# Kernel tuning notes

Measured on AMD Instinct MI355X. Metric: run time of the kernel, lower is better.

The kernel has to match this reference:

```python
import jax, jax.numpy as jnp
import numpy as np

B, T, C, H = 4, 2048, 1024, 16
D = C // H  # head dim = 64

def setup_inputs() -> dict:
    key = jax.random.key(0)
    k1, k2, k3 = jax.random.split(key, 3)
    x = jax.random.normal(k1, (B, T, C), dtype=jnp.float32)
    # torch Linear weight [out,in]; store transposed for x @ W
    W_attn = jax.random.normal(k2, (C, 3 * C), dtype=jnp.float32) * (1.0 / np.sqrt(C))
    W_proj = jax.random.normal(k3, (C, C), dtype=jnp.float32) * (1.0 / np.sqrt(C))
    return {"x": x, "W_attn": W_attn, "W_proj": W_proj}

def reference(x, W_attn, W_proj):
    qkv = x @ W_attn                          # [B,T,3C]
    q, k, v = jnp.split(qkv, 3, axis=-1)
    # [B,T,C] -> [B,H,T,D]
    def heads(t):
        return t.reshape(B, T, H, D).transpose(0, 2, 1, 3)
    q, k, v = heads(q), heads(k), heads(v)
    att = jnp.einsum('bhqd,bhkd->bhqk', q, k) * (1.0 / np.sqrt(D))  # [B,H,T,T]
    causal = jnp.tril(jnp.ones((T, T), dtype=bool))
    att = jnp.where(causal[None, None, :, :], att, -jnp.inf)
    att = jax.nn.softmax(att, axis=-1)
    y = jnp.einsum('bhqk,bhkd->bhqd', att, v)  # [B,H,T,D]
    y = y.transpose(0, 2, 1, 3).reshape(B, T, C)
    return y @ W_proj
```

## Files before the change

kernel.cpp:

```cpp
#include <hip/hip_runtime.h>
#include <hip/hip_bf16.h>

#define BB 4
#define TT 2048
#define CC 1024
#define HH 16
#define DD 64
#define MM (BB*TT)

typedef unsigned short u16;
typedef __bf16 bf16x8 __attribute__((ext_vector_type(8)));
typedef __bf16 bf16x4v __attribute__((ext_vector_type(4)));
typedef u16 u16x8 __attribute__((ext_vector_type(8)));
typedef u16 u16x4 __attribute__((ext_vector_type(4)));
typedef float f32x4 __attribute__((ext_vector_type(4)));

__device__ __forceinline__ u16 f2bf(float f) {
  union { float f; unsigned u; } v; v.f = f;
  unsigned u = v.u;
  return (u16)((u + 0x7fffu + ((u >> 16) & 1u)) >> 16);
}
__device__ __forceinline__ float bf2f(u16 s) {
  union { unsigned u; float f; } v; v.u = ((unsigned)s) << 16; return v.f;
}
__device__ __forceinline__ bf16x8 ld_bf16x8(const u16* p) {
  return *reinterpret_cast<const bf16x8*>(p);
}
__device__ __forceinline__ f32x4 zero4() {
  f32x4 z; z[0] = 0.f; z[1] = 0.f; z[2] = 0.f; z[3] = 0.f; return z;
}

__device__ __forceinline__ void gld_lds16(const u16* g, u16* l) {
  __builtin_amdgcn_global_load_lds(
      (const __attribute__((address_space(1))) void*)g,
      (__attribute__((address_space(3))) void*)l, 16, 0, 0);
}
__device__ __forceinline__ void wait_vm0() { __builtin_amdgcn_s_waitcnt(0x0F70); }

__device__ __forceinline__ float lane_pull(float x, int srclane) {
  int r = __builtin_amdgcn_ds_bpermute(srclane << 2, __builtin_bit_cast(int, x));
  return __builtin_bit_cast(float, r);
}

#define NC4B ((MM * CC / 4) / 256)
__global__ void k_prep(const float* __restrict__ x, u16* __restrict__ xb,
                       const float* __restrict__ Wa, u16* __restrict__ Wab,
                       const float* __restrict__ Wp, u16* __restrict__ Wpb) {
  __shared__ float tile[32][33];
  const int bx = blockIdx.x;
  if (bx < NC4B) {
    int i = bx * 256 + threadIdx.x;
    const float4 v = reinterpret_cast<const float4*>(x)[i];
    u16x4 r; r.x = f2bf(v.x); r.y = f2bf(v.y); r.z = f2bf(v.z); r.w = f2bf(v.w);
    reinterpret_cast<u16x4*>(xb)[i] = r;
    return;
  }
  const float* W; u16* Wt; int K, N, b2;
  if (bx < NC4B + 3072) { W = Wa; Wt = Wab; K = CC; N = 3 * CC; b2 = bx - NC4B; }
  else                  { W = Wp; Wt = Wpb; K = CC; N = CC;     b2 = bx - NC4B - 3072; }
  const int nblk = N / 32;
  const int nb = (b2 % nblk) * 32, kb = (b2 / nblk) * 32;
  const int tx = threadIdx.x & 31, ty = threadIdx.x >> 5;
  #pragma unroll
  for (int i = ty; i < 32; i += 8)
    tile[i][tx] = W[(size_t)(kb + i) * N + nb + tx];
  __syncthreads();
  #pragma unroll
  for (int i = ty; i < 32; i += 8)
    Wt[(size_t)(nb + i) * K + kb + tx] = f2bf(tile[tx][i]);
}

template<int EPI>
__global__ __launch_bounds__(256, 3)
void k_gemm_bt(const u16* __restrict__ A, const u16* __restrict__ Bt,
               float* __restrict__ outF, u16* __restrict__ qb, u16* __restrict__ kb,
               u16* __restrict__ vt, int N, int K)
{
  __shared__ u16 As[128 * 64];
  __shared__ u16 Bs[128 * 64];
  const int tid  = threadIdx.x;
  const int lane = tid & 63, w = tid >> 6;
  const int l16  = lane & 15, quad = lane >> 4;
  const int wr = w >> 1, wc = w & 1;
  const int m0 = blockIdx.y * 128, n0 = blockIdx.x * 128;
  const int lr8 = lane >> 3, lc8 = lane & 7;

  f32x4 acc[4][4];
  #pragma unroll
  for (int i = 0; i < 4; ++i)
    #pragma unroll
    for (int j = 0; j < 4; ++j) acc[i][j] = zero4();

  for (int k0 = 0; k0 < K; k0 += 64) {
    __syncthreads();
    #pragma unroll
    for (int p = 0; p < 4; ++p) {
      const int row = w * 32 + p * 8 + lr8;
      const int cs  = lc8 ^ (row & 7);
      gld_lds16(A  + (size_t)(m0 + row) * K + k0 + cs * 8, &As[(w * 32 + p * 8) * 64]);
      gld_lds16(Bt + (size_t)(n0 + row) * K + k0 + cs * 8, &Bs[(w * 32 + p * 8) * 64]);
    }
    wait_vm0();
    __syncthreads();
    #pragma unroll
    for (int s = 0; s < 2; ++s) {
      bf16x8 af[4], bfr[4];
      #pragma unroll
      for (int i = 0; i < 4; ++i) {
        int mrow = wr * 64 + i * 16 + l16;
        af[i]  = ld_bf16x8(&As[mrow * 64 + ((s * 4 + quad) ^ (l16 & 7)) * 8]);
        int nrow = wc * 64 + i * 16 + l16;
        bfr[i] = ld_bf16x8(&Bs[nrow * 64 + ((s * 4 + quad) ^ (l16 & 7)) * 8]);
      }
      #pragma unroll
      for (int i = 0; i < 4; ++i)
        #pragma unroll
        for (int j = 0; j < 4; ++j)
          acc[i][j] = __builtin_amdgcn_mfma_f32_16x16x32_bf16(af[i], bfr[j], acc[i][j], 0, 0, 0);
    }
  }

  #pragma unroll
  for (int i = 0; i < 4; ++i) {
    #pragma unroll
    for (int j = 0; j < 4; ++j) {
      const int n = n0 + wc * 64 + j * 16 + l16;
      const int mb = m0 + wr * 64 + i * 16 + quad * 4;
      if (EPI == 0) {
        #pragma unroll
        for (int r = 0; r < 4; ++r)
          outF[(size_t)(mb + r) * N + n] = acc[i][j][r];
      } else {
        const int b = mb >> 11, tb = mb & 2047;
        if (n < CC) {
          const int h = n >> 6, d = n & 63;
          #pragma unroll
          for (int r = 0; r < 4; ++r)
            qb[(((size_t)(b * HH + h) * TT + tb + r) << 6) + d] = f2bf(acc[i][j][r]);
        } else if (n < 2 * CC) {
          const int n2 = n - CC; const int h = n2 >> 6, d = n2 & 63;
          #pragma unroll
          for (int r = 0; r < 4; ++r)
            kb[(((size_t)(b * HH + h) * TT + tb + r) << 6) + d] = f2bf(acc[i][j][r]);
        } else {
          const int n2 = n - 2 * CC; const int h = n2 >> 6, d = n2 & 63;
          u16x4 cv;
          #pragma unroll
          for (int r = 0; r < 4; ++r) cv[r] = f2bf(acc[i][j][r]);
          *reinterpret_cast<u16x4*>(
              vt + ((size_t)(b * HH + h) * DD + d) * TT + tb) = cv;
        }
      }
    }
  }
}

__global__ __launch_bounds__(256, 4)
void k_attn(const u16* __restrict__ qb, const u16* __restrict__ kb,
            const u16* __restrict__ vt, u16* __restrict__ y)
{
  __shared__ u16 Ks[128 * 64];
  __shared__ u16 Vs[64 * 128];
  __shared__ u16 QP[64 * 64];
  const int tid  = threadIdx.x;
  const int lane = tid & 63, w = tid >> 6;
  const int l16  = lane & 15, quad = lane >> 4;
  const int lr8 = lane >> 3, lc8 = lane & 7;

  const int bx = blockIdx.x;
  const int qt = 31 - (bx >> 6);
  const int bh = bx & 63;
  const int h  = bh & 15, b = bh >> 4;

  const u16* qptr = qb + ((size_t)bh * TT + qt * 64) * DD;
  const u16* kptr = kb + (size_t)bh * TT * DD;
  const u16* vptr = vt + (size_t)bh * DD * TT;

  const float qscale = 0.125f * 1.44269504088896340736f;
  #pragma unroll
  for (int p = 0; p < 2; ++p) {
    const int r = w * 16 + p * 8 + lr8;
    u16x8 v = *reinterpret_cast<const u16x8*>(qptr + (size_t)r * DD + lc8 * 8);
    u16x8 o;
    #pragma unroll
    for (int e = 0; e < 8; ++e) o[e] = f2bf(bf2f(v[e]) * qscale);
    *reinterpret_cast<u16x8*>(&QP[r * 64 + (lc8 ^ lr8) * 8]) = o;
  }
  bf16x8 qf[2];
  #pragma unroll
  for (int s = 0; s < 2; ++s)
    qf[s] = ld_bf16x8(&QP[(w * 16 + l16) * 64 + ((s * 4 + quad) ^ (l16 & 7)) * 8]);

  float rsum = 0.f;
  f32x4 O[4];
  #pragma unroll
  for (int j = 0; j < 4; ++j) O[j] = zero4();

  const int qend = qt * 64;
  const int nkt  = (qt >> 1) + 1;
  for (int kt = 0; kt < nkt; ++kt) {
    __syncthreads();
    {
      const u16* kt0 = kptr + (size_t)kt * 128 * DD;
      #pragma unroll
      for (int p = 0; p < 4; ++p) {
        const int row = w * 32 + p * 8 + lr8;
        const int cs  = lc8 ^ (row & 7);
        gld_lds16(kt0 + (size_t)row * DD + cs * 8, &Ks[(w * 32 + p * 8) * 64]);
      }
      #pragma unroll
      for (int p = 0; p < 4; ++p) {
        const int d  = w * 16 + p * 4 + (lane >> 4);
        const int cs = (lane & 15) ^ (d & 7);
        gld_lds16(vptr + (size_t)d * TT + kt * 128 + cs * 8,
                  &Vs[(w * 16 + p * 4) * 128]);
      }
    }
    wait_vm0();
    __syncthreads();

    #pragma unroll
    for (int h2 = 0; h2 < 2; ++h2) {
      const int k0 = kt * 128 + h2 * 64;
      if (k0 <= qend) {
        f32x4 St[4];
        #pragma unroll
        for (int j = 0; j < 4; ++j) St[j] = zero4();
        #pragma unroll
        for (int s = 0; s < 2; ++s) {
          #pragma unroll
          for (int j = 0; j < 4; ++j) {
            bf16x8 kfr = ld_bf16x8(&Ks[(h2 * 64 + j * 16 + l16) * 64 +
                                       ((s * 4 + quad) ^ (l16 & 7)) * 8]);
            St[j] = __builtin_amdgcn_mfma_f32_16x16x32_bf16(kfr, qf[s], St[j], 0, 0, 0);
          }
        }
        if (k0 == qend) {
          const int qg = w * 16 + l16;
          #pragma unroll
          for (int j = 0; j < 4; ++j)
            #pragma unroll
            for (int r = 0; r < 4; ++r)
              if (j * 16 + quad * 4 + r > qg) St[j][r] = -__builtin_inff();
        }

        #pragma unroll
        for (int j = 0; j < 4; ++j)
          #pragma unroll
          for (int r = 0; r < 4; ++r) {
            float p = __builtin_amdgcn_exp2f(St[j][r]);
            St[j][r] = p;
            rsum += p;
          }

        #pragma unroll
        for (int j = 0; j < 4; ++j) {
          union { bf16x4v bv; u16x4 u; } cv;
          cv.bv[0] = (__bf16)St[j][0]; cv.bv[1] = (__bf16)St[j][1];
          cv.bv[2] = (__bf16)St[j][2]; cv.bv[3] = (__bf16)St[j][3];
          const int c = j * 2 + (quad >> 1);
          const int off = w * 1024 + l16 * 64 + ((c ^ (l16 & 7)) << 3) + ((quad & 1) << 2);
          *reinterpret_cast<u16x4*>(&QP[off]) = cv.u;
        }
        #pragma unroll
        for (int s = 0; s < 2; ++s) {
          bf16x8 pf = ld_bf16x8(&QP[w * 1024 + l16 * 64 +
                                    ((s * 4 + quad) ^ (l16 & 7)) * 8]);
          #pragma unroll
          for (int j = 0; j < 4; ++j) {
            bf16x8 vf = ld_bf16x8(&Vs[(j * 16 + l16) * 128 +
                                      ((h2 * 8 + s * 4 + quad) ^ (l16 & 7)) * 8]);
            O[j] = __builtin_amdgcn_mfma_f32_16x16x32_bf16(pf, vf, O[j], 0, 0, 0);
          }
        }
      }
    }
  }

  rsum += __shfl_xor(rsum, 16);
  rsum += __shfl_xor(rsum, 32);
  const float linv = 1.0f / rsum;
  f32x4 lv;
  #pragma unroll
  for (int r = 0; r < 4; ++r) lv[r] = lane_pull(linv, quad * 4 + r);
  #pragma unroll
  for (int j = 0; j < 4; ++j) {
    O[j] *= lv;
    #pragma unroll
    for (int r = 0; r < 4; ++r) {
      int t  = qt * 64 + w * 16 + quad * 4 + r;
      int ch = h * 64 + j * 16 + l16;
      y[(size_t)(b * TT + t) * CC + ch] = f2bf(O[j][r]);
    }
  }
}

extern "C" void kernel_launch(void* const* d_in, const int* in_sizes, int n_in,
                              void* d_out, int out_size, void* d_ws, size_t ws_size,
                              hipStream_t stream) {
  const float* x  = (const float*)d_in[0];
  const float* Wa = (const float*)d_in[1];
  const float* Wp = (const float*)d_in[2];
  float* out = (float*)d_out;

  u16* ws   = (u16*)d_ws;
  u16* xb   = ws;
  u16* Wab  = xb   + (size_t)MM * CC;
  u16* Wpb  = Wab  + (size_t)3 * CC * CC;
  u16* qbuf = Wpb  + (size_t)CC * CC;
  u16* kbuf = qbuf + (size_t)MM * CC;
  u16* vtb  = kbuf + (size_t)MM * CC;
  u16* yb   = vtb  + (size_t)MM * CC;

  k_prep<<<NC4B + 3072 + 1024, 256, 0, stream>>>(x, xb, Wa, Wab, Wp, Wpb);
  k_gemm_bt<1><<<dim3(3 * CC / 128, MM / 128), 256, 0, stream>>>(
      xb, Wab, nullptr, qbuf, kbuf, vtb, 3 * CC, CC);
  k_attn<<<64 * 32, 256, 0, stream>>>(qbuf, kbuf, vtb, yb);
  k_gemm_bt<0><<<dim3(CC / 128, MM / 128), 256, 0, stream>>>(
      yb, Wpb, out, nullptr, nullptr, nullptr, CC, CC);
}
```

Before: 243.4 us.

## Prefetch next K/V tile into registers to overlap global loads with compute

Replaces the direct global-to-LDS loads, which waited on vmcnt(0) every iteration, with a register-staged software pipeline. The next K/V tile is loaded into registers while the current tile is written to LDS and computed on. This hides global memory latency behind the MFMA work. In exchange it costs extra VGPRs, which may reduce occupancy, and it relies on raw s_barrier plus manual lgkmcnt waits for correctness.

```diff
diff --git a/kernel.cpp b/kernel.cpp
--- a/kernel.cpp
+++ b/kernel.cpp
@@ -176,6 +176,22 @@
   const u16* kptr = kb + (size_t)bh * TT * DD;
   const u16* vptr = vt + (size_t)bh * DD * TT;
 
+  const int krow = w * 32 + lr8;
+  const u16* kgp = kptr + (size_t)krow * DD + lc8 * 8;
+  const int vd = w * 16 + (lane >> 4);
+  const u16* vgp = vptr + (size_t)vd * TT + (lane & 15) * 8;
+
+  const int qend = qt * 64;
+  const int nkt  = (qt >> 1) + 1;
+
+  int4 kr[4], vr[4];
+  #pragma unroll
+  for (int p = 0; p < 4; ++p)
+    kr[p] = *reinterpret_cast<const int4*>(kgp + (size_t)(p * 8) * DD);
+  #pragma unroll
+  for (int p = 0; p < 4; ++p)
+    vr[p] = *reinterpret_cast<const int4*>(vgp + (size_t)(p * 4) * TT);
+
   const float qscale = 0.125f * 1.44269504088896340736f;
   #pragma unroll
   for (int p = 0; p < 2; ++p) {
@@ -196,28 +212,29 @@
   #pragma unroll
   for (int j = 0; j < 4; ++j) O[j] = zero4();
 
-  const int qend = qt * 64;
-  const int nkt  = (qt >> 1) + 1;
   for (int kt = 0; kt < nkt; ++kt) {
-    __syncthreads();
-    {
-      const u16* kt0 = kptr + (size_t)kt * 128 * DD;
+    __builtin_amdgcn_s_barrier();
+    #pragma unroll
+    for (int p = 0; p < 4; ++p) {
+      const int row = w * 32 + p * 8 + lr8;
+      *reinterpret_cast<int4*>(&Ks[row * 64 + ((lc8 ^ (row & 7)) << 3)]) = kr[p];
+    }
+    #pragma unroll
+    for (int p = 0; p < 4; ++p) {
+      const int d = vd + p * 4;
+      *reinterpret_cast<int4*>(&Vs[d * 128 + (((lane & 15) ^ (d & 7)) << 3)]) = vr[p];
+    }
+    if (kt + 1 < nkt) {
+      const size_t ko = (size_t)(kt + 1) * 128;
       #pragma unroll
-      for (int p = 0; p < 4; ++p) {
-        const int row = w * 32 + p * 8 + lr8;
-        const int cs  = lc8 ^ (row & 7);
-        gld_lds16(kt0 + (size_t)row * DD + cs * 8, &Ks[(w * 32 + p * 8) * 64]);
-      }
+      for (int p = 0; p < 4; ++p)
+        kr[p] = *reinterpret_cast<const int4*>(kgp + (ko + (size_t)(p * 8)) * DD);
       #pragma unroll
-      for (int p = 0; p < 4; ++p) {
-        const int d  = w * 16 + p * 4 + (lane >> 4);
-        const int cs = (lane & 15) ^ (d & 7);
-        gld_lds16(vptr + (size_t)d * TT + kt * 128 + cs * 8,
-                  &Vs[(w * 16 + p * 4) * 128]);
-      }
-    }
-    wait_vm0();
-    __syncthreads();
+      for (int p = 0; p < 4; ++p)
+        vr[p] = *reinterpret_cast<const int4*>(vgp + ko + (size_t)(p * 4) * TT);
+    }
+    asm volatile("s_waitcnt lgkmcnt(0)" ::: "memory");
+    __builtin_amdgcn_s_barrier();
 
     #pragma unroll
     for (int h2 = 0; h2 < 2; ++h2) {
```

Result: slower. 350.5 us (+44.0%).

## Process 128 query rows per attention block to reuse K/V tiles across two groups

Applied to the files above, without the earlier changes.

The attention kernel now handles 128 query rows per block (two 64-row groups per wave) instead of 64, so each K/V tile loaded into shared memory feeds twice as many MFMAs and the grid is halved. Q staging temporarily reuses the Ks buffer, and the P scratch buffer is doubled. The intent is to cut the redundant global-to-LDS K/V traffic across blocks. In exchange register pressure rises (launch bounds lowered to 3 blocks per CU), there are fewer blocks to balance the causal workload, and on the last tile the group-0 half is skipped, leaving some idle work.

```diff
diff --git a/kernel.cpp b/kernel.cpp
--- a/kernel.cpp
+++ b/kernel.cpp
@@ -155,49 +155,51 @@
   }
 }
 
-__global__ __launch_bounds__(256, 4)
+__global__ __launch_bounds__(256, 3)
 void k_attn(const u16* __restrict__ qb, const u16* __restrict__ kb,
             const u16* __restrict__ vt, u16* __restrict__ y)
 {
   __shared__ u16 Ks[128 * 64];
   __shared__ u16 Vs[64 * 128];
-  __shared__ u16 QP[64 * 64];
+  __shared__ u16 QP[8 * 1024];
   const int tid  = threadIdx.x;
   const int lane = tid & 63, w = tid >> 6;
   const int l16  = lane & 15, quad = lane >> 4;
   const int lr8 = lane >> 3, lc8 = lane & 7;
 
   const int bx = blockIdx.x;
-  const int qt = 31 - (bx >> 6);
+  const int qt = 15 - (bx >> 6);
   const int bh = bx & 63;
   const int h  = bh & 15, b = bh >> 4;
 
-  const u16* qptr = qb + ((size_t)bh * TT + qt * 64) * DD;
+  const u16* qptr = qb + ((size_t)bh * TT + qt * 128) * DD;
   const u16* kptr = kb + (size_t)bh * TT * DD;
   const u16* vptr = vt + (size_t)bh * DD * TT;
 
   const float qscale = 0.125f * 1.44269504088896340736f;
   #pragma unroll
-  for (int p = 0; p < 2; ++p) {
-    const int r = w * 16 + p * 8 + lr8;
+  for (int p = 0; p < 4; ++p) {
+    const int r = w * 32 + p * 8 + lr8;
     u16x8 v = *reinterpret_cast<const u16x8*>(qptr + (size_t)r * DD + lc8 * 8);
     u16x8 o;
     #pragma unroll
     for (int e = 0; e < 8; ++e) o[e] = f2bf(bf2f(v[e]) * qscale);
-    *reinterpret_cast<u16x8*>(&QP[r * 64 + (lc8 ^ lr8) * 8]) = o;
-  }
-  bf16x8 qf[2];
-  #pragma unroll
-  for (int s = 0; s < 2; ++s)
-    qf[s] = ld_bf16x8(&QP[(w * 16 + l16) * 64 + ((s * 4 + quad) ^ (l16 & 7)) * 8]);
-
-  float rsum = 0.f;
-  f32x4 O[4];
-  #pragma unroll
-  for (int j = 0; j < 4; ++j) O[j] = zero4();
-
-  const int qend = qt * 64;
-  const int nkt  = (qt >> 1) + 1;
+    *reinterpret_cast<u16x8*>(&Ks[r * 64 + (lc8 ^ lr8) * 8]) = o;
+  }
+  __syncthreads();
+  bf16x8 qf0[2], qf1[2];
+  #pragma unroll
+  for (int s = 0; s < 2; ++s) {
+    qf0[s] = ld_bf16x8(&Ks[(w * 16 + l16) * 64 + ((s * 4 + quad) ^ (l16 & 7)) * 8]);
+    qf1[s] = ld_bf16x8(&Ks[(64 + w * 16 + l16) * 64 + ((s * 4 + quad) ^ (l16 & 7)) * 8]);
+  }
+
+  float rsum0 = 0.f, rsum1 = 0.f;
+  f32x4 O0[4], O1[4];
+  #pragma unroll
+  for (int j = 0; j < 4; ++j) { O0[j] = zero4(); O1[j] = zero4(); }
+
+  const int nkt = qt + 1;
   for (int kt = 0; kt < nkt; ++kt) {
     __syncthreads();
     {
@@ -205,7 +207,7 @@
       #pragma unroll
       for (int p = 0; p < 4; ++p) {
         const int row = w * 32 + p * 8 + lr8;
-        const int cs  = lc8 ^ (row & 7);
+        const int cs  = lc8 ^ lr8;
         gld_lds16(kt0 + (size_t)row * DD + cs * 8, &Ks[(w * 32 + p * 8) * 64]);
       }
       #pragma unroll
@@ -221,76 +223,120 @@
 
     #pragma unroll
     for (int h2 = 0; h2 < 2; ++h2) {
-      const int k0 = kt * 128 + h2 * 64;
-      if (k0 <= qend) {
-        f32x4 St[4];
-        #pragma unroll
-        for (int j = 0; j < 4; ++j) St[j] = zero4();
-        #pragma unroll
-        for (int s = 0; s < 2; ++s) {
-          #pragma unroll
-          for (int j = 0; j < 4; ++j) {
-            bf16x8 kfr = ld_bf16x8(&Ks[(h2 * 64 + j * 16 + l16) * 64 +
-                                       ((s * 4 + quad) ^ (l16 & 7)) * 8]);
-            St[j] = __builtin_amdgcn_mfma_f32_16x16x32_bf16(kfr, qf[s], St[j], 0, 0, 0);
-          }
-        }
-        if (k0 == qend) {
-          const int qg = w * 16 + l16;
+      const int  last = (kt == qt);
+      const bool g0on = !(last && h2 == 1);
+      f32x4 St0[4], St1[4];
+      #pragma unroll
+      for (int j = 0; j < 4; ++j) { St0[j] = zero4(); St1[j] = zero4(); }
+      #pragma unroll
+      for (int s = 0; s < 2; ++s) {
+        bf16x8 kfr[4];
+        #pragma unroll
+        for (int j = 0; j < 4; ++j)
+          kfr[j] = ld_bf16x8(&Ks[(h2 * 64 + j * 16 + l16) * 64 +
+                                 ((s * 4 + quad) ^ (l16 & 7)) * 8]);
+        if (g0on) {
+          #pragma unroll
+          for (int j = 0; j < 4; ++j)
+            St0[j] = __builtin_amdgcn_mfma_f32_16x16x32_bf16(kfr[j], qf0[s], St0[j], 0, 0, 0);
+        }
+        #pragma unroll
+        for (int j = 0; j < 4; ++j)
+          St1[j] = __builtin_amdgcn_mfma_f32_16x16x32_bf16(kfr[j], qf1[s], St1[j], 0, 0, 0);
+      }
+      if (last) {
+        const int qg = w * 16 + l16;
+        if (h2 == 0) {
           #pragma unroll
           for (int j = 0; j < 4; ++j)
             #pragma unroll
             for (int r = 0; r < 4; ++r)
-              if (j * 16 + quad * 4 + r > qg) St[j][r] = -__builtin_inff();
-        }
-
+              if (j * 16 + quad * 4 + r > qg) St0[j][r] = -__builtin_inff();
+        } else {
+          #pragma unroll
+          for (int j = 0; j < 4; ++j)
+            #pragma unroll
+            for (int r = 0; r < 4; ++r)
+              if (j * 16 + quad * 4 + r > qg) St1[j][r] = -__builtin_inff();
+        }
+      }
+
+      if (g0on) {
         #pragma unroll
         for (int j = 0; j < 4; ++j)
           #pragma unroll
           for (int r = 0; r < 4; ++r) {
-            float p = __builtin_amdgcn_exp2f(St[j][r]);
-            St[j][r] = p;
-            rsum += p;
+            float p = __builtin_amdgcn_exp2f(St0[j][r]);
+            St0[j][r] = p; rsum0 += p;
           }
-
         #pragma unroll
         for (int j = 0; j < 4; ++j) {
           union { bf16x4v bv; u16x4 u; } cv;
-          cv.bv[0] = (__bf16)St[j][0]; cv.bv[1] = (__bf16)St[j][1];
-          cv.bv[2] = (__bf16)St[j][2]; cv.bv[3] = (__bf16)St[j][3];
+          cv.bv[0] = (__bf16)St0[j][0]; cv.bv[1] = (__bf16)St0[j][1];
+          cv.bv[2] = (__bf16)St0[j][2]; cv.bv[3] = (__bf16)St0[j][3];
           const int c = j * 2 + (quad >> 1);
-          const int off = w * 1024 + l16 * 64 + ((c ^ (l16 & 7)) << 3) + ((quad & 1) << 2);
+          const int off = (w * 2 + 0) * 1024 + l16 * 64 +
+                          ((c ^ (l16 & 7)) << 3) + ((quad & 1) << 2);
           *reinterpret_cast<u16x4*>(&QP[off]) = cv.u;
         }
-        #pragma unroll
-        for (int s = 0; s < 2; ++s) {
-          bf16x8 pf = ld_bf16x8(&QP[w * 1024 + l16 * 64 +
-                                    ((s * 4 + quad) ^ (l16 & 7)) * 8]);
-          #pragma unroll
-          for (int j = 0; j < 4; ++j) {
-            bf16x8 vf = ld_bf16x8(&Vs[(j * 16 + l16) * 128 +
-                                      ((h2 * 8 + s * 4 + quad) ^ (l16 & 7)) * 8]);
-            O[j] = __builtin_amdgcn_mfma_f32_16x16x32_bf16(pf, vf, O[j], 0, 0, 0);
-          }
-        }
-      }
-    }
-  }
-
-  rsum += __shfl_xor(rsum, 16);
-  rsum += __shfl_xor(rsum, 32);
-  const float linv = 1.0f / rsum;
-  f32x4 lv;
-  #pragma unroll
-  for (int r = 0; r < 4; ++r) lv[r] = lane_pull(linv, quad * 4 + r);
-  #pragma unroll
-  for (int j = 0; j < 4; ++j) {
-    O[j] *= lv;
-    #pragma unroll
-    for (int r = 0; r < 4; ++r) {
-      int t  = qt * 64 + w * 16 + quad * 4 + r;
-      int ch = h * 64 + j * 16 + l16;
-      y[(size_t)(b * TT + t) * CC + ch] = f2bf(O[j][r]);
+      }
+      #pragma unroll
+      for (int j = 0; j < 4; ++j)
+        #pragma unroll
+        for (int r = 0; r < 4; ++r) {
+          float p = __builtin_amdgcn_exp2f(St1[j][r]);
+          St1[j][r] = p; rsum1 += p;
+        }
+      #pragma unroll
+      for (int j = 0; j < 4; ++j) {
+        union { bf16x4v bv; u16x4 u; } cv;
+        cv.bv[0] = (__bf16)St1[j][0]; cv.bv[1] = (__bf16)St1[j][1];
+        cv.bv[2] = (__bf16)St1[j][2]; cv.bv[3] = (__bf16)St1[j][3];
+        const int c = j * 2 + (quad >> 1);
+        const int off = (w * 2 + 1) * 1024 + l16 * 64 +
+                        ((c ^ (l16 & 7)) << 3) + ((quad & 1) << 2);
+        *reinterpret_cast<u16x4*>(&QP[off]) = cv.u;
+      }
+
+      #pragma unroll
+      for (int s = 0; s < 2; ++s) {
+        bf16x8 pf0, pf1;
+        if (g0on)
+          pf0 = ld_bf16x8(&QP[(w * 2 + 0) * 1024 + l16 * 64 +
+                              ((s * 4 + quad) ^ (l16 & 7)) * 8]);
+        pf1 = ld_bf16x8(&QP[(w * 2 + 1) * 1024 + l16 * 64 +
+                            ((s * 4 + quad) ^ (l16 & 7)) * 8]);
+        #pragma unroll
+        for (int j = 0; j < 4; ++j) {
+          bf16x8 vf = ld_bf16x8(&Vs[(j * 16 + l16) * 128 +
+                                    ((h2 * 8 + s * 4 + quad) ^ (l16 & 7)) * 8]);
+          if (g0on)
+            O0[j] = __builtin_amdgcn_mfma_f32_16x16x32_bf16(pf0, vf, O0[j], 0, 0, 0);
+          O1[j] = __builtin_amdgcn_mfma_f32_16x16x32_bf16(pf1, vf, O1[j], 0, 0, 0);
+        }
+      }
+    }
+  }
+
+  #pragma unroll
+  for (int g = 0; g < 2; ++g) {
+    float rs = (g == 0) ? rsum0 : rsum1;
+    rs += __shfl_xor(rs, 16);
+    rs += __shfl_xor(rs, 32);
+    const float linv = 1.0f / rs;
+    f32x4 lv;
+    #pragma unroll
+    for (int r = 0; r < 4; ++r) lv[r] = lane_pull(linv, quad * 4 + r);
+    #pragma unroll
+    for (int j = 0; j < 4; ++j) {
+      f32x4 o = (g == 0) ? O0[j] : O1[j];
+      o *= lv;
+      #pragma unroll
+      for (int r = 0; r < 4; ++r) {
+        int t  = qt * 128 + g * 64 + w * 16 + quad * 4 + r;
+        int ch = h * 64 + j * 16 + l16;
+        y[(size_t)(b * TT + t) * CC + ch] = f2bf(o[r]);
+      }
     }
   }
 }
@@ -315,7 +361,7 @@
   k_prep<<<NC4B + 3072 + 1024, 256, 0, stream>>>(x, xb, Wa, Wab, Wp, Wpb);
   k_gemm_bt<1><<<dim3(3 * CC / 128, MM / 128), 256, 0, stream>>>(
       xb, Wab, nullptr, qbuf, kbuf, vtb, 3 * CC, CC);
-  k_attn<<<64 * 32, 256, 0, stream>>>(qbuf, kbuf, vtb, yb);
+  k_attn<<<64 * 16, 256, 0, stream>>>(qbuf, kbuf, vtb, yb);
   k_gemm_bt<0><<<dim3(CC / 128, MM / 128), 256, 0, stream>>>(
       yb, Wpb, out, nullptr, nullptr, nullptr, CC, CC);
 }
```

Result: faster. 214.9 us, median of 2 (-11.7%).
